# Performance work log

Hardware: AMD Instinct MI355X
Metric: run time of the kernel (lower is better)

The kernel has to match this reference:

```python
import jax, jax.numpy as jnp
import numpy as np
import math

M = 0.5
S = 64.0
COS_M = math.cos(M)
SIN_M = math.sin(M)
MIN_COS = math.cos(math.pi - M)
NUM_CLASSES = 100000


def _l2norm(x, eps=1e-12):
    # matches F.normalize: x / max(||x||, eps)
    n = jnp.sqrt(jnp.sum(x * x, axis=-1, keepdims=True))
    return x / jnp.maximum(n, eps)


def setup_inputs() -> dict:
    key = jax.random.key(0)
    k1, k2, k3 = jax.random.split(key, 3)
    feats = jax.random.normal(k1, (8, 128, 512), dtype=jnp.float32)
    w = jax.random.normal(k2, (NUM_CLASSES, 512), dtype=jnp.float32)
    labels = jax.random.randint(k3, (1024,), 0, NUM_CLASSES, dtype=jnp.int32)
    return {"feats": feats, "w": w, "labels": labels}


def reference(feats, w, labels):
    d = feats.shape[-1]
    f = _l2norm(feats).reshape(-1, d)          # [N, d]
    wn = _l2norm(w)                            # [C, d]
    cos_theta = jnp.clip(jnp.einsum('nd,cd->nc', f, wn), -1.0, 1.0)  # [N, C]
    sin_theta = jnp.sqrt(1.0 - cos_theta * cos_theta + 1e-5)
    cos_theta_m = cos_theta * COS_M - sin_theta * SIN_M
    target_logit = jnp.where(cos_theta > MIN_COS, cos_theta_m,
                             cos_theta - sin_theta * M)
    # apply margin only at the label column
    onehot = jax.nn.one_hot(labels, cos_theta.shape[1], dtype=cos_theta.dtype)
    logits = (onehot * target_logit + (1.0 - onehot) * cos_theta) * S
    logp = jax.nn.log_softmax(logits, axis=-1)
    nll = -jnp.take_along_axis(logp, labels[:, None].astype(jnp.int32), axis=1)[:, 0]
    return jnp.mean(nll)
```

## Files before the change

### kernel.cpp

```cpp
#include <hip/hip_runtime.h>
#include <hip/hip_bf16.h>
#include <stdint.h>

#define NUM_CLASSES 100000
#define C_PAD       100096
#define NROWS       1024
#define KDIM        512
#define BM          128
#define BN          128
#define BK          32
#define NKT         (KDIM / BK)
#define TILE_BYTES  8192
#define RB_BYTES    (NKT * TILE_BYTES)
#define RB_U16      (RB_BYTES / 2)

#define L2E64 92.3324826f

typedef __bf16 bf16x8 __attribute__((ext_vector_type(8)));
typedef float  f32x4  __attribute__((ext_vector_type(4)));
typedef unsigned short u16x8 __attribute__((ext_vector_type(8)));

__device__ __forceinline__ unsigned short f2bf(float x) {
    unsigned int u = __float_as_uint(x);
    u = u + 0x7fffu + ((u >> 16) & 1u);
    return (unsigned short)(u >> 16);
}
__device__ __forceinline__ float bf2f(unsigned short x) {
    return __uint_as_float(((unsigned int)x) << 16);
}
__device__ __forceinline__ float fexp64(float c) {
    return exp2f(fmaf(c, L2E64, -L2E64));
}
__device__ __forceinline__ void gload_lds16(const void* g, void* l) {
    __builtin_amdgcn_global_load_lds(
        (const __attribute__((address_space(1))) unsigned int*)g,
        (__attribute__((address_space(3))) unsigned int*)l,
        16, 0, 0);
}


__global__ void norm_rows_tiled(const float* __restrict__ in,
                                unsigned short* __restrict__ out,
                                int rows_valid, int rows_total) {
    const int lane = threadIdx.x & 63;
    const int row  = blockIdx.x * 4 + (threadIdx.x >> 6);
    if (row >= rows_total) return;
    unsigned short* dst = out + (size_t)(row >> 7) * RB_U16
                              + (lane >> 2) * 4096 + (lane & 3) * 1024
                              + (row & 127) * 8;
    if (row >= rows_valid) {
        u16x8 z;
        #pragma unroll
        for (int i = 0; i < 8; ++i) z[i] = 0;
        *(u16x8*)dst = z;
        return;
    }
    const float4* p = (const float4*)(in + (size_t)row * KDIM + lane * 8);
    float4 a = p[0], b = p[1];
    float ss = a.x*a.x + a.y*a.y + a.z*a.z + a.w*a.w
             + b.x*b.x + b.y*b.y + b.z*b.z + b.w*b.w;
    #pragma unroll
    for (int m = 1; m < 64; m <<= 1) ss += __shfl_xor(ss, m, 64);
    float scale = 1.0f / fmaxf(sqrtf(ss), 1e-12f);
    float v[8] = {a.x, a.y, a.z, a.w, b.x, b.y, b.z, b.w};
    u16x8 o;
    #pragma unroll
    for (int i = 0; i < 8; ++i) o[i] = f2bf(v[i] * scale);
    *(u16x8*)dst = o;
}

__global__ __launch_bounds__(256) void arcface_gemm(
        const unsigned short* __restrict__ fbT,
        const unsigned short* __restrict__ wbT,
        float* __restrict__ rowsum) {
    __shared__ __align__(16) unsigned short ldsA[BM * BK];
    __shared__ __align__(16) unsigned short ldsB[BN * BK];
    __shared__ float lds_rs[BM];

    const int tid  = threadIdx.x;
    const int lane = tid & 63;
    const int wid  = tid >> 6;
    const int wr   = wid >> 1;
    const int wc   = wid & 1;
    const int l15  = lane & 15;
    const int kg   = lane >> 4;

    const int wgid = (blockIdx.x & 7) * 782 + (blockIdx.x >> 3);
    const int colb = wgid >> 3;
    const int mrow = wgid & 7;
    const int row0 = mrow * BM;
    const int col0 = colb * BN;

    const char* aBase = (const char*)fbT + (size_t)mrow * RB_BYTES;
    const char* bBase = (const char*)wbT + (size_t)colb * RB_BYTES;

    f32x4 acc[4][4];
    #pragma unroll
    for (int m = 0; m < 4; ++m)
        #pragma unroll
        for (int n = 0; n < 4; ++n)
            #pragma unroll
            for (int j = 0; j < 4; ++j) acc[m][n][j] = 0.f;

    const int o0 = tid * 16;

    for (int kt = 0; kt < NKT; ++kt) {
        __syncthreads();
        const char* aT = aBase + kt * TILE_BYTES;
        const char* bT = bBase + kt * TILE_BYTES;
        #pragma unroll
        for (int c = 0; c < 2; ++c) {
            const int o = o0 + c * 4096;
            gload_lds16(aT + o, (char*)ldsA + o);
            gload_lds16(bT + o, (char*)ldsB + o);
        }
        __syncthreads();

        bf16x8 af[4], bfr[4];
        #pragma unroll
        for (int m = 0; m < 4; ++m) {
            const int rr = wr * 64 + m * 16 + l15;
            af[m] = *(const bf16x8*)((const char*)ldsA + kg * 2048 + rr * 16);
        }
        #pragma unroll
        for (int n = 0; n < 4; ++n) {
            const int cr = wc * 64 + n * 16 + l15;
            bfr[n] = *(const bf16x8*)((const char*)ldsB + kg * 2048 + cr * 16);
        }
        #pragma unroll
        for (int m = 0; m < 4; ++m)
            #pragma unroll
            for (int n = 0; n < 4; ++n)
                acc[m][n] = __builtin_amdgcn_mfma_f32_16x16x32_bf16(
                                af[m], bfr[n], acc[m][n], 0, 0, 0);
    }

    if (tid < BM) lds_rs[tid] = 0.f;
    __syncthreads();

    float rs[4][4];
    #pragma unroll
    for (int m = 0; m < 4; ++m)
        #pragma unroll
        for (int j = 0; j < 4; ++j) rs[m][j] = 0.f;

    #pragma unroll
    for (int n = 0; n < 4; ++n) {
        const int colg = col0 + wc * 64 + n * 16 + l15;
        const bool valid = colg < NUM_CLASSES;
        #pragma unroll
        for (int m = 0; m < 4; ++m) {
            #pragma unroll
            for (int j = 0; j < 4; ++j) {
                float c = acc[m][n][j];
                c = fminf(fmaxf(c, -1.f), 1.f);
                float t = fexp64(c);
                rs[m][j] += valid ? t : 0.f;
            }
        }
    }
    #pragma unroll
    for (int m = 0; m < 4; ++m) {
        #pragma unroll
        for (int j = 0; j < 4; ++j) {
            float v = rs[m][j];
            v += __shfl_xor(v, 1, 64);
            v += __shfl_xor(v, 2, 64);
            v += __shfl_xor(v, 4, 64);
            v += __shfl_xor(v, 8, 64);
            rs[m][j] = v;
        }
    }
    if (l15 == 0) {
        #pragma unroll
        for (int m = 0; m < 4; ++m)
            #pragma unroll
            for (int j = 0; j < 4; ++j)
                atomicAdd(&lds_rs[wr * 64 + m * 16 + kg * 4 + j], rs[m][j]);
    }
    __syncthreads();
    if (tid < BM) atomicAdd(&rowsum[row0 + tid], lds_rs[tid]);
}

__global__ void label_dot(const unsigned short* __restrict__ fbT,
                          const unsigned short* __restrict__ wbT,
                          const int* __restrict__ labels,
                          float* __restrict__ coslab) {
    const int lane = threadIdx.x & 63;
    const int row  = blockIdx.x * 4 + (threadIdx.x >> 6);
    if (row >= NROWS) return;
    const int lab = labels[row];
    const size_t fo = (size_t)(row >> 7) * RB_U16 + (lane >> 2) * 4096
                    + (lane & 3) * 1024 + (row & 127) * 8;
    const size_t wo = (size_t)(lab >> 7) * RB_U16 + (lane >> 2) * 4096
                    + (lane & 3) * 1024 + (lab & 127) * 8;
    u16x8 a = *(const u16x8*)(fbT + fo);
    u16x8 b = *(const u16x8*)(wbT + wo);
    float s = 0.f;
    #pragma unroll
    for (int i = 0; i < 8; ++i) s = fmaf(bf2f(a[i]), bf2f(b[i]), s);
    #pragma unroll
    for (int m = 1; m < 64; m <<= 1) s += __shfl_xor(s, m, 64);
    if (lane == 0) coslab[row] = s;
}

__global__ void finalize(const float* __restrict__ rowsum,
                         const float* __restrict__ coslab,
                         float* __restrict__ out) {
    const float COS_M   =  0.87758256189f;
    const float SIN_M   =  0.47942553860f;
    const float MIN_COS = -0.87758256189f;
    __shared__ float red[256];
    const int tid = threadIdx.x;
    float acc = 0.f;
    for (int r = tid; r < NROWS; r += 256) {
        float c = fminf(fmaxf(coslab[r], -1.f), 1.f);
        float sn = sqrtf(1.f - c * c + 1e-5f);
        float cm = c * COS_M - sn * SIN_M;
        float target = (c > MIN_COS) ? cm : (c - sn * 0.5f);
        float adj = rowsum[r] - fexp64(c) + fexp64(target);
        acc += 64.f + logf(adj) - 64.f * target;
    }
    red[tid] = acc;
    __syncthreads();
    for (int s = 128; s > 0; s >>= 1) {
        if (tid < s) red[tid] += red[tid + s];
        __syncthreads();
    }
    if (tid == 0) out[0] = red[0] / (float)NROWS;
}

extern "C" void kernel_launch(void* const* d_in, const int* in_sizes, int n_in,
                              void* d_out, int out_size, void* d_ws, size_t ws_size,
                              hipStream_t stream) {
    const float* feats  = (const float*)d_in[0];
    const float* w      = (const float*)d_in[1];
    const int*   labels = (const int*)d_in[2];
    float* out = (float*)d_out;

    char* ws = (char*)d_ws;
    unsigned short* wbT = (unsigned short*)ws;
    unsigned short* fbT = (unsigned short*)(ws + (size_t)C_PAD * KDIM * 2);
    float* rowsum = (float*)(ws + (size_t)C_PAD * KDIM * 2
                                + (size_t)NROWS * KDIM * 2);
    float* coslab = rowsum + NROWS;

    hipMemsetAsync(rowsum, 0, NROWS * sizeof(float), stream);
    norm_rows_tiled<<<C_PAD / 4, 256, 0, stream>>>(w, wbT, NUM_CLASSES, C_PAD);
    norm_rows_tiled<<<NROWS / 4, 256, 0, stream>>>(feats, fbT, NROWS, NROWS);
    arcface_gemm<<<(C_PAD / BN) * (NROWS / BM), 256, 0, stream>>>(fbT, wbT, rowsum);
    label_dot<<<NROWS / 4, 256, 0, stream>>>(fbT, wbT, labels, coslab);
    finalize<<<1, 256, 0, stream>>>(rowsum, coslab, out);
}
```

Before: 475.7 us.

## Double-buffer GEMM LDS tiles and coalesce normalized-weight writes via LDS staging

The GEMM now keeps two LDS buffers for A and B. It prefetches the next K tile with global_load_lds while running MFMAs on the current one, which cuts the per-iteration barriers from two to one. The row-normalization kernel stages its bf16 output in shared memory and transposes it, so each global store writes contiguous 64-byte runs instead of scattered 16-byte pieces. The padded-column mask in the softmax epilogue is dropped, relying on zero padding rows giving a negligible exp(-64) term. This doubles GEMM LDS usage, which may affect occupancy.

```diff
diff --git a/kernel.cpp b/kernel.cpp
--- a/kernel.cpp
+++ b/kernel.cpp
@@ -41,40 +41,46 @@
 
 __global__ void norm_rows_tiled(const float* __restrict__ in,
                                 unsigned short* __restrict__ out,
-                                int rows_valid, int rows_total) {
-    const int lane = threadIdx.x & 63;
-    const int row  = blockIdx.x * 4 + (threadIdx.x >> 6);
-    if (row >= rows_total) return;
-    unsigned short* dst = out + (size_t)(row >> 7) * RB_U16
-                              + (lane >> 2) * 4096 + (lane & 3) * 1024
-                              + (row & 127) * 8;
-    if (row >= rows_valid) {
-        u16x8 z;
-        #pragma unroll
-        for (int i = 0; i < 8; ++i) z[i] = 0;
-        *(u16x8*)dst = z;
-        return;
-    }
-    const float4* p = (const float4*)(in + (size_t)row * KDIM + lane * 8);
-    float4 a = p[0], b = p[1];
-    float ss = a.x*a.x + a.y*a.y + a.z*a.z + a.w*a.w
-             + b.x*b.x + b.y*b.y + b.z*b.z + b.w*b.w;
-    #pragma unroll
-    for (int m = 1; m < 64; m <<= 1) ss += __shfl_xor(ss, m, 64);
-    float scale = 1.0f / fmaxf(sqrtf(ss), 1e-12f);
-    float v[8] = {a.x, a.y, a.z, a.w, b.x, b.y, b.z, b.w};
+                                int rows_valid) {
+    __shared__ __align__(16) unsigned short stg[4 * 64 * 8];
+    const int tid  = threadIdx.x;
+    const int lane = tid & 63;
+    const int wv   = tid >> 6;
+    const int row  = blockIdx.x * 4 + wv;
+
     u16x8 o;
     #pragma unroll
-    for (int i = 0; i < 8; ++i) o[i] = f2bf(v[i] * scale);
-    *(u16x8*)dst = o;
+    for (int i = 0; i < 8; ++i) o[i] = 0;
+    if (row < rows_valid) {
+        const float4* p = (const float4*)(in + (size_t)row * KDIM + lane * 8);
+        float4 a = p[0], b = p[1];
+        float ss = a.x*a.x + a.y*a.y + a.z*a.z + a.w*a.w
+                 + b.x*b.x + b.y*b.y + b.z*b.z + b.w*b.w;
+        #pragma unroll
+        for (int m = 1; m < 64; m <<= 1) ss += __shfl_xor(ss, m, 64);
+        float scale = 1.0f / fmaxf(sqrtf(ss), 1e-12f);
+        float v[8] = {a.x, a.y, a.z, a.w, b.x, b.y, b.z, b.w};
+        #pragma unroll
+        for (int i = 0; i < 8; ++i) o[i] = f2bf(v[i] * scale);
+    }
+    *(u16x8*)&stg[(wv * 64 + lane) * 8] = o;
+    __syncthreads();
+
+    const int c    = tid >> 2;
+    const int r4   = tid & 3;
+    const int rowg = blockIdx.x * 4 + r4;
+    u16x8 v = *(const u16x8*)&stg[(r4 * 64 + c) * 8];
+    const size_t dst = (size_t)(rowg >> 7) * RB_U16
+                     + (c >> 2) * 4096 + (c & 3) * 1024 + (rowg & 127) * 8;
+    *(u16x8*)(out + dst) = v;
 }
 
 __global__ __launch_bounds__(256) void arcface_gemm(
         const unsigned short* __restrict__ fbT,
         const unsigned short* __restrict__ wbT,
         float* __restrict__ rowsum) {
-    __shared__ __align__(16) unsigned short ldsA[BM * BK];
-    __shared__ __align__(16) unsigned short ldsB[BN * BK];
+    __shared__ __align__(16) unsigned short ldsA[2][BM * BK];
+    __shared__ __align__(16) unsigned short ldsB[2][BN * BK];
     __shared__ float lds_rs[BM];
 
     const int tid  = threadIdx.x;
@@ -89,7 +95,6 @@
     const int colb = wgid >> 3;
     const int mrow = wgid & 7;
     const int row0 = mrow * BM;
-    const int col0 = colb * BN;
 
     const char* aBase = (const char*)fbT + (size_t)mrow * RB_BYTES;
     const char* bBase = (const char*)wbT + (size_t)colb * RB_BYTES;
@@ -104,28 +109,37 @@
 
     const int o0 = tid * 16;
 
+    #pragma unroll
+    for (int ch = 0; ch < 2; ++ch) {
+        const int o = o0 + ch * 4096;
+        gload_lds16(aBase + o, (char*)ldsA[0] + o);
+        gload_lds16(bBase + o, (char*)ldsB[0] + o);
+    }
+    __syncthreads();
+
+    int cur = 0;
     for (int kt = 0; kt < NKT; ++kt) {
-        __syncthreads();
-        const char* aT = aBase + kt * TILE_BYTES;
-        const char* bT = bBase + kt * TILE_BYTES;
-        #pragma unroll
-        for (int c = 0; c < 2; ++c) {
-            const int o = o0 + c * 4096;
-            gload_lds16(aT + o, (char*)ldsA + o);
-            gload_lds16(bT + o, (char*)ldsB + o);
-        }
-        __syncthreads();
+        if (kt + 1 < NKT) {
+            const char* aT = aBase + (kt + 1) * TILE_BYTES;
+            const char* bT = bBase + (kt + 1) * TILE_BYTES;
+            #pragma unroll
+            for (int ch = 0; ch < 2; ++ch) {
+                const int o = o0 + ch * 4096;
+                gload_lds16(aT + o, (char*)ldsA[cur ^ 1] + o);
+                gload_lds16(bT + o, (char*)ldsB[cur ^ 1] + o);
+            }
+        }
 
         bf16x8 af[4], bfr[4];
         #pragma unroll
         for (int m = 0; m < 4; ++m) {
             const int rr = wr * 64 + m * 16 + l15;
-            af[m] = *(const bf16x8*)((const char*)ldsA + kg * 2048 + rr * 16);
+            af[m] = *(const bf16x8*)((const char*)ldsA[cur] + kg * 2048 + rr * 16);
         }
         #pragma unroll
         for (int n = 0; n < 4; ++n) {
             const int cr = wc * 64 + n * 16 + l15;
-            bfr[n] = *(const bf16x8*)((const char*)ldsB + kg * 2048 + cr * 16);
+            bfr[n] = *(const bf16x8*)((const char*)ldsB[cur] + kg * 2048 + cr * 16);
         }
         #pragma unroll
         for (int m = 0; m < 4; ++m)
@@ -133,6 +147,9 @@
             for (int n = 0; n < 4; ++n)
                 acc[m][n] = __builtin_amdgcn_mfma_f32_16x16x32_bf16(
                                 af[m], bfr[n], acc[m][n], 0, 0, 0);
+
+        __syncthreads();
+        cur ^= 1;
     }
 
     if (tid < BM) lds_rs[tid] = 0.f;
@@ -146,16 +163,13 @@
 
     #pragma unroll
     for (int n = 0; n < 4; ++n) {
-        const int colg = col0 + wc * 64 + n * 16 + l15;
-        const bool valid = colg < NUM_CLASSES;
         #pragma unroll
         for (int m = 0; m < 4; ++m) {
             #pragma unroll
             for (int j = 0; j < 4; ++j) {
                 float c = acc[m][n][j];
                 c = fminf(fmaxf(c, -1.f), 1.f);
-                float t = fexp64(c);
-                rs[m][j] += valid ? t : 0.f;
+                rs[m][j] += fexp64(c);
             }
         }
     }
@@ -246,8 +260,8 @@
     float* coslab = rowsum + NROWS;
 
     hipMemsetAsync(rowsum, 0, NROWS * sizeof(float), stream);
-    norm_rows_tiled<<<C_PAD / 4, 256, 0, stream>>>(w, wbT, NUM_CLASSES, C_PAD);
-    norm_rows_tiled<<<NROWS / 4, 256, 0, stream>>>(feats, fbT, NROWS, NROWS);
+    norm_rows_tiled<<<C_PAD / 4, 256, 0, stream>>>(w, wbT, NUM_CLASSES);
+    norm_rows_tiled<<<NROWS / 4, 256, 0, stream>>>(feats, fbT, NROWS);
     arcface_gemm<<<(C_PAD / BN) * (NROWS / BM), 256, 0, stream>>>(fbT, wbT, rowsum);
     label_dot<<<NROWS / 4, 256, 0, stream>>>(fbT, wbT, labels, coslab);
     finalize<<<1, 256, 0, stream>>>(rowsum, coslab, out);
```

Result: faster. 465.4 us (-2.2%).
